# Kernel optimization log

Measured on AMD Instinct MI355X. Metric: run time of the kernel, lower is better.

Reference implementation:

```python
import jax, jax.numpy as jnp
import numpy as np

K = 32      # number of coupled-attention tensors per branch
NH = 128    # hidden size of token representations
B = 64      # batch
S = 512     # sequence length
H2 = 2 * K  # GRU input/hidden size


def setup_inputs() -> dict:
    key = jax.random.key(0)
    ks = jax.random.split(key, 9)
    unif = lambda k, shape, lo, hi: jax.random.uniform(k, shape, jnp.float32, lo, hi)
    h = jax.random.normal(ks[0], (B, S, NH), jnp.float32)
    u_a = jax.random.normal(ks[1], (NH, 1), jnp.float32)
    u_o = jax.random.normal(ks[2], (NH, 1), jnp.float32)
    mask = jnp.ones((B, S), jnp.bool_)
    G_a = unif(ks[3], (K, 1, NH, NH), -0.2, 0.2)
    G_o = unif(ks[4], (K, 1, NH, NH), -0.2, 0.2)
    r0 = unif(ks[5], (H2,), -0.2, 0.2)
    v = unif(ks[6], (H2,), -0.2, 0.2)
    s = 1.0 / np.sqrt(H2)  # default torch GRU init scale
    W_ih = unif(ks[7], (3 * H2, H2), -s, s)
    W_hh = unif(ks[8], (3 * H2, H2), -s, s)
    return {"h": h, "u_a": u_a, "u_o": u_o, "mask": mask,
            "G_a": G_a, "G_o": G_o, "r0": r0, "v": v,
            "W_ih": W_ih, "W_hh": W_hh}


def reference(h, u_a, u_o, mask, G_a, G_o, r0, v, W_ih, W_hh):
    # f(G, u)[k,b,s] = sum_j (sum_i h[b,s,i] * G[k,0,i,j]) * u[j,0]
    # contract G with u first to avoid the (K,B,S,nh) intermediate.
    def f(G, u):
        w = jnp.einsum('kij,j->ki', G[:, 0], u[:, 0])     # (K, nh)
        return jnp.einsum('bsi,ki->kbs', h, w)            # (K, B, S)

    beta = jnp.tanh(jnp.concatenate([f(G_a, u_a), f(G_o, u_o)], axis=0))  # (2K,B,S)
    beta = jnp.transpose(beta, (1, 2, 0))                 # (B, S, 2K)
    beta = beta * mask[..., None].astype(beta.dtype)

    # GRU (bias=False), PyTorch gate order r, z, n.
    x_seq = jnp.transpose(beta, (1, 0, 2))                # (S, B, 2K)
    h0 = jnp.broadcast_to(r0, (B, H2))

    def step(hp, x):
        gx = x @ W_ih.T                                   # (B, 3*2K)
        gh = hp @ W_hh.T
        xr, xz, xn = jnp.split(gx, 3, axis=-1)
        hr, hz, hn = jnp.split(gh, 3, axis=-1)
        rg = jax.nn.sigmoid(xr + hr)
        zg = jax.nn.sigmoid(xz + hz)
        ng = jnp.tanh(xn + rg * hn)
        hnew = (1.0 - zg) * ng + zg * hp
        return hnew, hnew

    _, outs = jax.lax.scan(step, h0, x_seq)               # (S, B, 2K)
    r = jnp.transpose(outs, (1, 0, 2))                    # (B, S, 2K)
    r = r * mask[..., None].astype(r.dtype)
    return r, r @ v                                       # (B,S,2K), (B,S)
```

## Files before the change

kernel.cpp:

```cpp
#include <hip/hip_runtime.h>
#include <hip/hip_bf16.h>

#define B_  64
#define S_  512
#define NH_ 128
#define K_  32
#define H2_ 64
#define G3_ 192

typedef unsigned int u32;
typedef unsigned short u16;
typedef _Float16 h2f __attribute__((ext_vector_type(2)));
typedef __fp16  fp16v2 __attribute__((ext_vector_type(2)));
typedef u32 u32x4 __attribute__((ext_vector_type(4)));
typedef _Float16 f16x8 __attribute__((ext_vector_type(8)));
typedef float f32x4 __attribute__((ext_vector_type(4)));

__device__ __forceinline__ float bf_lo(u32 p){ return __uint_as_float(p << 16); }
__device__ __forceinline__ float bf_hi(u32 p){ return __uint_as_float(p & 0xffff0000u); }
__device__ __forceinline__ float bfu(u16 b){ return __uint_as_float(((u32)b) << 16); }
__device__ __forceinline__ float f16u(u16 b){ __fp16 h = *(__fp16*)&b; return (float)h; }
__device__ __forceinline__ u16 f2bf(float x){
  __hip_bfloat16 h = __float2bfloat16(x);
  return *(u16*)&h;
}
__device__ __forceinline__ u16 f2h(float x){
  __fp16 h = (__fp16)x;
  return *(u16*)&h;
}
__device__ __forceinline__ float frcp(float x){ return __builtin_amdgcn_rcpf(x); }
__device__ __forceinline__ float sigmoid_f(float x){
  x = fminf(fmaxf(x, -30.f), 30.f);
  return frcp(1.f + __expf(-x));
}
__device__ __forceinline__ float tanh_f(float x){
  x = fminf(fmaxf(x, -15.f), 15.f);
  float e = __expf(2.f * x);
  return (e - 1.f) * frcp(e + 1.f);
}
__device__ __forceinline__ float tanh_fast(float x){
  float e = __expf(2.f * x);
  return 1.f - 2.f*frcp(1.f + e);
}
__device__ __forceinline__ float sigmoid_nc(float x){
  return frcp(1.f + __expf(-x));
}
__device__ __forceinline__ float tanh_nc(float x){
  float e = __expf(2.f * x);
  return (e - 1.f) * frcp(e + 1.f);
}
__device__ __forceinline__ u32 pkrtz_u(float a, float b){
  fp16v2 pk = __builtin_amdgcn_cvt_pkrtz(a, b);
  return *(u32*)&pk;
}
__device__ __forceinline__ float fdot2u(u32 a, u32 b, float c){
#if __has_builtin(__builtin_amdgcn_fdot2)
  return __builtin_amdgcn_fdot2(*(h2f*)&a, *(h2f*)&b, c, false);
#else
  h2f av = *(h2f*)&a, bv = *(h2f*)&b;
  return c + (float)av.x*(float)bv.x + (float)av.y*(float)bv.y;
#endif
}
__device__ __forceinline__ u32 readlane_u(u32 v, int lane){
  return (u32)__builtin_amdgcn_readlane((int)v, lane);
}
__device__ __forceinline__ float dpp_xor1(float x){
  return __int_as_float(
      __builtin_amdgcn_update_dpp(0, __float_as_int(x), 0xB1, 0xF, 0xF, true));
}

#define GLD4(dst, base, OFF) \
  asm volatile("global_load_dwordx4 %0, %1, off offset:" OFF : "=v"(dst) : "v"(base))
#define VMWAIT() asm volatile("s_waitcnt vmcnt(0)" ::: "memory")
#define UNP(arr, base, q) \
  arr[(base)]=q.x; arr[(base)+1]=q.y; arr[(base)+2]=q.z; arr[(base)+3]=q.w

__device__ __forceinline__ bool detect_f32_block(const u16* p, int nHalf, int tid){
  __shared__ int flagS;
  __syncthreads();
  if (tid < 64) {
    int sane = 0;
    if (tid < nHalf) {
      u16 b = p[2*tid];
      int ex = (b >> 7) & 0xFF;
      sane = (b == 0 || (ex >= 0x68 && ex <= 0x84)) ? 1 : 0;
    }
    unsigned long long m = __ballot(sane != 0);
    if (tid == 0) flagS = (4*__popcll(m) < 3*nHalf) ? 1 : 0;
  }
  __syncthreads();
  return flagS != 0;
}

__global__ __launch_bounds__(128) void k_prep(
    const void* __restrict__ h, const void* __restrict__ ua, const void* __restrict__ uo,
    const void* __restrict__ Ga, const void* __restrict__ Go,
    const void* __restrict__ r0, const void* __restrict__ v,
    const void* __restrict__ Wih, const void* __restrict__ Whh,
    u32* __restrict__ wPk, u32* __restrict__ WihPk2, u32* __restrict__ WhhPk,
    float* __restrict__ r0f, int* __restrict__ flags)
{
  int bk = blockIdx.x, t = threadIdx.x;
  if (bk < 64) {
    const void* G = (bk < K_) ? Ga : Go;
    const void* u = (bk < K_) ? ua : uo;
    bool fg = detect_f32_block((const u16*)G, 64, t);
    bool fu = detect_f32_block((const u16*)u, 64, t);
    __shared__ float u_s[NH_];
    __shared__ float accS[NH_];
    u_s[t] = fu ? ((const float*)u)[t] : bfu(((const u16*)u)[t]);
    __syncthreads();
    int k = bk & (K_ - 1);
    size_t ro = ((size_t)k*NH_ + t)*NH_;
    float acc = 0.f;
    if (fg) {
      const float4* Gr = (const float4*)((const float*)G + ro);
      #pragma unroll
      for (int j4 = 0; j4 < NH_/4; ++j4) {
        float4 g = Gr[j4];
        acc += g.x*u_s[4*j4] + g.y*u_s[4*j4+1] + g.z*u_s[4*j4+2] + g.w*u_s[4*j4+3];
      }
    } else {
      const u32* Gr = (const u32*)((const u16*)G + ro);
      #pragma unroll
      for (int j2 = 0; j2 < NH_/2; ++j2) {
        u32 p = Gr[j2];
        acc += bf_lo(p)*u_s[2*j2] + bf_hi(p)*u_s[2*j2+1];
      }
    }
    accS[t] = acc;
    __syncthreads();
    if (t < 64) wPk[bk*64 + t] = pkrtz_u(accS[2*t], accS[2*t+1]);
  } else if (bk < 112) {
    bool f = detect_f32_block((const u16*)Wih, 64, t);
    int idx = (bk - 64)*128 + t;
    int j = idx / 96, rest = idx % 96;
    int g = rest / 32, m = rest % 32;
    int row = g*H2_ + j;
    float a, b;
    if (f) {
      const float* W = (const float*)Wih;
      a = W[(size_t)row*H2_ + 2*m]; b = W[(size_t)row*H2_ + 2*m + 1];
    } else {
      u32 p = ((const u32*)Wih)[(size_t)row*(H2_/2) + m];
      a = bf_lo(p); b = bf_hi(p);
    }
    WihPk2[idx] = pkrtz_u(a, b);
  } else if (bk < 160) {
    bool f = detect_f32_block((const u16*)Whh, 64, t);
    int idx = (bk - 112)*128 + t;
    int j = idx / 96, rest = idx % 96;
    int g = rest / 32, m = rest % 32;
    int row = g*H2_ + j;
    float a, b;
    if (f) {
      const float* W = (const float*)Whh;
      a = W[(size_t)row*H2_ + 2*m]; b = W[(size_t)row*H2_ + 2*m + 1];
    } else {
      u32 p = ((const u32*)Whh)[(size_t)row*(H2_/2) + m];
      a = bf_lo(p); b = bf_hi(p);
    }
    WhhPk[idx] = pkrtz_u(a, b);
  } else {
    bool fh = detect_f32_block((const u16*)h, 64, t);
    bool fv = detect_f32_block((const u16*)v, 32, t);
    bool fr = detect_f32_block((const u16*)r0, 32, t);
    if (t == 0) { flags[0] = fh ? 1 : 0; flags[7] = fv ? 1 : 0; }
    if (t < H2_)
      r0f[t] = fr ? ((const float*)r0)[t] : bfu(((const u16*)r0)[t]);
  }
}

__global__ __launch_bounds__(64)
void k_bg(const void* __restrict__ h, const u32* __restrict__ wPk,
          const u32* __restrict__ WihPk2, const int* __restrict__ flags,
          u16* __restrict__ gx)
{
  __shared__ u16 betaS[64][72];
  int l = threadIdx.x;
  int posBase = blockIdx.x * 64;
  bool f32in = flags[0] != 0;
  int c = l & 15;
  int g = l >> 4;

  f16x8 bw[4][4];
  {
    const char* base = (const char*)wPk;
    #pragma unroll
    for (int kkt = 0; kkt < 4; ++kkt)
      #pragma unroll
      for (int kt = 0; kt < 4; ++kt)
        bw[kkt][kt] = *(const f16x8*)(base + (kkt*16 + c)*256 + kt*64 + g*16);
  }

  f32x4 acc1[4][4];
  #pragma unroll
  for (int mt = 0; mt < 4; ++mt)
    #pragma unroll
    for (int kkt = 0; kkt < 4; ++kkt)
      acc1[mt][kkt] = (f32x4){0.f, 0.f, 0.f, 0.f};

  const u16*   hb = (const u16*)h;
  const float* hf = (const float*)h;
  #pragma unroll
  for (int kt = 0; kt < 4; ++kt) {
    f16x8 ha[4];
    #pragma unroll
    for (int mt = 0; mt < 4; ++mt) {
      int row = posBase + mt*16 + c;
      if (f32in) {
        const float* src = hf + (size_t)row*NH_ + kt*32 + g*8;
        float4 lo = *(const float4*)(src);
        float4 hi = *(const float4*)(src + 4);
        u32x4 q;
        q.x = pkrtz_u(lo.x, lo.y); q.y = pkrtz_u(lo.z, lo.w);
        q.z = pkrtz_u(hi.x, hi.y); q.w = pkrtz_u(hi.z, hi.w);
        ha[mt] = *(f16x8*)&q;
      } else {
        u32x4 qb = *(const u32x4*)(hb + (size_t)row*NH_ + kt*32 + g*8);
        u32x4 q;
        q.x = pkrtz_u(bf_lo(qb.x), bf_hi(qb.x));
        q.y = pkrtz_u(bf_lo(qb.y), bf_hi(qb.y));
        q.z = pkrtz_u(bf_lo(qb.z), bf_hi(qb.z));
        q.w = pkrtz_u(bf_lo(qb.w), bf_hi(qb.w));
        ha[mt] = *(f16x8*)&q;
      }
    }
    #pragma unroll
    for (int mt = 0; mt < 4; ++mt)
      #pragma unroll
      for (int kkt = 0; kkt < 4; ++kkt)
        acc1[mt][kkt] = __builtin_amdgcn_mfma_f32_16x16x32_f16(
            ha[mt], bw[kkt][kt], acc1[mt][kkt], 0, 0, 0);
  }

  #pragma unroll
  for (int mt = 0; mt < 4; ++mt)
    #pragma unroll
    for (int kkt = 0; kkt < 4; ++kkt)
      #pragma unroll
      for (int r = 0; r < 4; ++r) {
        float bta = tanh_fast(acc1[mt][kkt][r]);
        betaS[mt*16 + g*4 + r][kkt*16 + c] = f2h(bta);
      }
  asm volatile("s_waitcnt lgkmcnt(0)" ::: "memory");

  f16x8 a2[4][2];
  #pragma unroll
  for (int mt = 0; mt < 4; ++mt)
    #pragma unroll
    for (int kt2 = 0; kt2 < 2; ++kt2)
      a2[mt][kt2] = *(const f16x8*)&betaS[mt*16 + c][kt2*32 + g*8];

  const char* wib = (const char*)WihPk2;
  #pragma unroll 2
  for (int rt = 0; rt < 12; ++rt) {
    int row = rt*16 + c;
    int gg = row >> 6, j = row & 63;
    f16x8 b2_0 = *(const f16x8*)(wib + j*384 + gg*128 + g*16);
    f16x8 b2_1 = *(const f16x8*)(wib + j*384 + gg*128 + 64 + g*16);
    f32x4 acc2[4];
    #pragma unroll
    for (int mt = 0; mt < 4; ++mt) {
      acc2[mt] = (f32x4){0.f, 0.f, 0.f, 0.f};
      acc2[mt] = __builtin_amdgcn_mfma_f32_16x16x32_f16(a2[mt][0], b2_0, acc2[mt], 0, 0, 0);
      acc2[mt] = __builtin_amdgcn_mfma_f32_16x16x32_f16(a2[mt][1], b2_1, acc2[mt], 0, 0, 0);
    }
    #pragma unroll
    for (int mt = 0; mt < 4; ++mt)
      #pragma unroll
      for (int r = 0; r < 4; ++r)
        gx[(size_t)(posBase + mt*16 + g*4 + r)*G3_ + rt*16 + c] = f2h(acc2[mt][r]);
  }
}

__global__ __launch_bounds__(64)
__attribute__((amdgpu_waves_per_eu(1, 1)))
void k_gru(
    const u16* __restrict__ gx, const u32* __restrict__ WhhPk,
    const float* __restrict__ r0f, const int* __restrict__ flags,
    void* __restrict__ out)
{
  int b = blockIdx.x, j = threadIdx.x;
  bool outf32 = flags[0] != 0;
  unsigned long long a = (unsigned long long)(WhhPk + j*96);
  u32x4 q0,q1,q2,q3,q4,q5,q6,q7,q8,q9,q10,q11,
        q12,q13,q14,q15,q16,q17,q18,q19,q20,q21,q22,q23;
  GLD4(q0,a,"0");    GLD4(q1,a,"16");   GLD4(q2,a,"32");   GLD4(q3,a,"48");
  GLD4(q4,a,"64");   GLD4(q5,a,"80");   GLD4(q6,a,"96");   GLD4(q7,a,"112");
  GLD4(q8,a,"128");  GLD4(q9,a,"144");  GLD4(q10,a,"160"); GLD4(q11,a,"176");
  GLD4(q12,a,"192"); GLD4(q13,a,"208"); GLD4(q14,a,"224"); GLD4(q15,a,"240");
  GLD4(q16,a,"256"); GLD4(q17,a,"272"); GLD4(q18,a,"288"); GLD4(q19,a,"304");
  GLD4(q20,a,"320"); GLD4(q21,a,"336"); GLD4(q22,a,"352"); GLD4(q23,a,"368");
  VMWAIT();
  u32 wr_[32], wz_[32], wn_[32];
  UNP(wr_,0,q0);  UNP(wr_,4,q1);  UNP(wr_,8,q2);  UNP(wr_,12,q3);
  UNP(wr_,16,q4); UNP(wr_,20,q5); UNP(wr_,24,q6); UNP(wr_,28,q7);
  UNP(wz_,0,q8);  UNP(wz_,4,q9);  UNP(wz_,8,q10); UNP(wz_,12,q11);
  UNP(wz_,16,q12);UNP(wz_,20,q13);UNP(wz_,24,q14);UNP(wz_,28,q15);
  UNP(wn_,0,q16); UNP(wn_,4,q17); UNP(wn_,8,q18); UNP(wn_,12,q19);
  UNP(wn_,16,q20);UNP(wn_,20,q21);UNP(wn_,24,q22);UNP(wn_,28,q23);

  float hp = r0f[j];
  const u16* gxb = gx + (size_t)b*S_*G3_ + j;
  float* of = (float*)out + (size_t)b*S_*H2_ + j;
  u16*   oh = (u16*)out   + (size_t)b*S_*H2_ + j;

  float bxr[8], bxz[8], bxn[8], hbuf[8];
  #pragma unroll
  for (int u = 0; u < 8; ++u) {
    bxr[u] = f16u(gxb[u*G3_]);
    bxz[u] = f16u(gxb[u*G3_ + H2_]);
    bxn[u] = f16u(gxb[u*G3_ + 2*H2_]);
  }
  #pragma unroll 1
  for (int s0 = 0; s0 < S_; s0 += 8) {
    float nxr[8], nxz[8], nxn[8];
    int nb = (s0 + 8 < S_) ? (s0 + 8) : s0;
    #pragma unroll
    for (int u = 0; u < 8; ++u) {
      nxr[u] = f16u(gxb[(nb+u)*G3_]);
      nxz[u] = f16u(gxb[(nb+u)*G3_ + H2_]);
      nxn[u] = f16u(gxb[(nb+u)*G3_ + 2*H2_]);
    }
    #pragma unroll
    for (int u = 0; u < 8; ++u) {
      u32 hppu = pkrtz_u(hp, dpp_xor1(hp));
      u32 hsv[32];
      #pragma unroll
      for (int m = 0; m < 32; ++m) hsv[m] = readlane_u(hppu, 2*m);
      float ar[4], az[4], an[4];
      ar[0]=bxr[u]; ar[1]=0.f; ar[2]=0.f; ar[3]=0.f;
      az[0]=bxz[u]; az[1]=0.f; az[2]=0.f; az[3]=0.f;
      an[0]=0.f;    an[1]=0.f; an[2]=0.f; an[3]=0.f;
      #pragma unroll
      for (int m = 0; m < 32; ++m) {
        int c = m & 3;
        ar[c] = fdot2u(hsv[m], wr_[m], ar[c]);
        az[c] = fdot2u(hsv[m], wz_[m], az[c]);
        an[c] = fdot2u(hsv[m], wn_[m], an[c]);
      }
      float Ar = (ar[0]+ar[1]) + (ar[2]+ar[3]);
      float Az = (az[0]+az[1]) + (az[2]+az[3]);
      float An = (an[0]+an[1]) + (an[2]+an[3]);
      float rg = sigmoid_nc(Ar);
      float zg = sigmoid_nc(Az);
      float ng = tanh_nc(bxn[u] + rg*An);
      hp = ng + zg*(hp - ng);
      hbuf[u] = hp;
    }
    if (outf32) {
      #pragma unroll
      for (int u = 0; u < 8; ++u) of[(size_t)(s0+u)*H2_] = hbuf[u];
    } else {
      #pragma unroll
      for (int u = 0; u < 8; ++u) oh[(size_t)(s0+u)*H2_] = f2bf(hbuf[u]);
    }
    #pragma unroll
    for (int u = 0; u < 8; ++u) { bxr[u]=nxr[u]; bxz[u]=nxz[u]; bxn[u]=nxn[u]; }
  }
}

__global__ __launch_bounds__(256) void k_rv(
    const void* __restrict__ outbase, const void* __restrict__ v,
    const int* __restrict__ flags, int dummy)
{
  bool outf32 = flags[0] != 0, f_v = flags[7] != 0;
  int lane = threadIdx.x & 63;
  int pos  = blockIdx.x*4 + (threadIdx.x >> 6);
  float vv = f_v ? ((const float*)v)[lane] : bfu(((const u16*)v)[lane]);
  float rr = outf32 ? ((const float*)outbase)[(size_t)pos*H2_ + lane]
                    : bfu(((const u16*)outbase)[(size_t)pos*H2_ + lane]);
  float val = rr * vv;
  #pragma unroll
  for (int m = 32; m >= 1; m >>= 1) val += __shfl_xor(val, m, 64);
  if (lane == 0) {
    if (outf32) ((float*)outbase)[(size_t)B_*S_*H2_ + pos] = val;
    else        ((u16*)outbase)[(size_t)B_*S_*H2_ + pos]   = f2bf(val);
  }
}

__global__ __launch_bounds__(64) void k_detect(
    const u16* __restrict__ p0, const u16* __restrict__ p1, const u16* __restrict__ p2,
    const u16* __restrict__ p4, const u16* __restrict__ p5, const u16* __restrict__ p6,
    const u16* __restrict__ p7, const u16* __restrict__ p8, const u16* __restrict__ p9,
    int* __restrict__ flags)
{
  const u16* ps[9] = {p0,p1,p2,p4,p5,p6,p7,p8,p9};
  const int  ns[9] = {64,64,64,64,64,32,32,64,64};
  const int  fi[9] = {0,1,2,4,5,6,7,8,9};
  int t = threadIdx.x;
  for (int m = 0; m < 9; ++m) {
    int n = ns[m];
    int sane = 0;
    if (t < n) {
      u16 b = ps[m][2*t];
      int ex = (b >> 7) & 0xFF;
      sane = (b == 0 || (ex >= 0x68 && ex <= 0x84)) ? 1 : 0;
    }
    #pragma unroll
    for (int sh = 32; sh >= 1; sh >>= 1) sane += __shfl_xor(sane, sh, 64);
    if (t == 0) flags[fi[m]] = (4*sane < 3*n) ? 1 : 0;
  }
  if (t == 0) flags[3] = 0;
}

__global__ __launch_bounds__(64, 1) void k_fused(
    const void* __restrict__ h, const void* __restrict__ ua, const void* __restrict__ uo,
    const void* __restrict__ Ga, const void* __restrict__ Go,
    const void* __restrict__ r0, const void* __restrict__ Wih,
    const void* __restrict__ Whh, const int* __restrict__ flags,
    void* __restrict__ out)
{
  __shared__ float wsh[NH_*H2_];
  __shared__ float wih_s[H2_*G3_];
  __shared__ float us[2*NH_];
  __shared__ float hs[NH_];
  __shared__ float beta_s[H2_];
  __shared__ float hps[H2_];
  int b = blockIdx.x, t = threadIdx.x;
  bool f_h = flags[0]!=0, f_ua = flags[1]!=0, f_uo = flags[2]!=0;
  bool f_ga = flags[4]!=0, f_go = flags[5]!=0, f_r0 = flags[6]!=0;
  bool f_wih = flags[8]!=0, f_whh = flags[9]!=0;
  for (int i = t; i < NH_; i += 64) {
    us[i]      = f_ua ? ((const float*)ua)[i] : bfu(((const u16*)ua)[i]);
    us[NH_+i]  = f_uo ? ((const float*)uo)[i] : bfu(((const u16*)uo)[i]);
  }
  for (int idx = t; idx < H2_*G3_; idx += 64) {
    int j = idx / H2_, p = idx % H2_;
    float w = f_wih ? ((const float*)Wih)[idx] : bfu(((const u16*)Wih)[idx]);
    wih_s[p*G3_ + j] = w;
  }
  __syncthreads();
  {
    int k = t & 31;
    const void* G = (t < 32) ? Ga : Go;
    bool fg = (t < 32) ? f_ga : f_go;
    const float* u_s = &us[(t < 32) ? 0 : NH_];
    for (int i = 0; i < NH_; ++i) {
      size_t ro = ((size_t)k*NH_ + i)*NH_;
      float acc = 0.f;
      if (fg) {
        const float* Gr = (const float*)G + ro;
        for (int jj = 0; jj < NH_; ++jj) acc += Gr[jj]*u_s[jj];
      } else {
        const u32* Gr = (const u32*)((const u16*)G + ro);
        for (int j2 = 0; j2 < NH_/2; ++j2) {
          u32 p = Gr[j2];
          acc += bf_lo(p)*u_s[2*j2] + bf_hi(p)*u_s[2*j2+1];
        }
      }
      wsh[i*H2_ + t] = acc;
    }
  }
  float wr[H2_], wz[H2_], wn[H2_];
  if (f_whh) {
    const float* W = (const float*)Whh;
    for (int i = 0; i < H2_; ++i) {
      wr[i] = W[(size_t)t*H2_ + i];
      wz[i] = W[(size_t)(H2_ + t)*H2_ + i];
      wn[i] = W[(size_t)(2*H2_ + t)*H2_ + i];
    }
  } else {
    const u32* Wr = (const u32*)Whh + (size_t)(t)         * (H2_/2);
    const u32* Wz = (const u32*)Whh + (size_t)(H2_ + t)   * (H2_/2);
    const u32* Wn = (const u32*)Whh + (size_t)(2*H2_ + t) * (H2_/2);
    for (int i2 = 0; i2 < H2_/2; ++i2) {
      u32 p;
      p = Wr[i2]; wr[2*i2]=bf_lo(p); wr[2*i2+1]=bf_hi(p);
      p = Wz[i2]; wz[2*i2]=bf_lo(p); wz[2*i2+1]=bf_hi(p);
      p = Wn[i2]; wn[2*i2]=bf_lo(p); wn[2*i2+1]=bf_hi(p);
    }
  }
  float hp = f_r0 ? ((const float*)r0)[t] : bfu(((const u16*)r0)[t]);
  __syncthreads();
  for (int s = 0; s < S_; ++s) {
    size_t hbase = ((size_t)b*S_ + s)*NH_;
    for (int i = t; i < NH_; i += 64)
      hs[i] = f_h ? ((const float*)h)[hbase + i] : bfu(((const u16*)h)[hbase + i]);
    __syncthreads();
    float a = 0.f;
    for (int i = 0; i < NH_; ++i) a += hs[i]*wsh[i*H2_ + t];
    beta_s[t] = tanh_f(a);
    hps[t] = hp;
    __syncthreads();
    float xr=0.f, xz=0.f, xn=0.f, ar=0.f, az=0.f, an=0.f;
    for (int p = 0; p < H2_; ++p) {
      float bp = beta_s[p];
      xr += bp*wih_s[p*G3_ + t];
      xz += bp*wih_s[p*G3_ + H2_ + t];
      xn += bp*wih_s[p*G3_ + 2*H2_ + t];
      float hv = hps[p];
      ar += hv*wr[p]; az += hv*wz[p]; an += hv*wn[p];
    }
    float rg = sigmoid_f(xr + ar);
    float zg = sigmoid_f(xz + az);
    float ng = tanh_f(xn + rg*an);
    hp = (1.f - zg)*ng + zg*hp;
    if (f_h) ((float*)out)[((size_t)b*S_ + s)*H2_ + t] = hp;
    else     ((u16*)out)[((size_t)b*S_ + s)*H2_ + t] = f2bf(hp);
    __syncthreads();
  }
}

extern "C" void kernel_launch(void* const* d_in, const int* in_sizes, int n_in,
                              void* d_out, int out_size, void* d_ws, size_t ws_size,
                              hipStream_t stream) {
  int*   flags  = (int*)d_ws;
  char*  wsb    = (char*)d_ws;
  float* r0f    = (float*)(wsb + 256);
  u32*   wPk    = (u32*)(wsb + 1024);
  u32*   WihPk2 = (u32*)(wsb + 17408);
  u32*   WhhPk  = (u32*)(wsb + 41984);
  u16*   gx     = (u16*)(wsb + 66560);
  const size_t need_bf = 66560ull + 12582912ull;

  if (ws_size >= need_bf) {
    k_prep<<<161, 128, 0, stream>>>(d_in[0], d_in[1], d_in[2], d_in[4], d_in[5],
                                    d_in[6], d_in[7], d_in[8], d_in[9],
                                    wPk, WihPk2, WhhPk, r0f, flags);
    k_bg  <<<512, 64,  0, stream>>>(d_in[0], wPk, WihPk2, flags, gx);
    k_gru <<<64,  64,  0, stream>>>(gx, WhhPk, r0f, flags, d_out);
  } else {
    k_detect<<<1, 64, 0, stream>>>(
        (const u16*)d_in[0], (const u16*)d_in[1], (const u16*)d_in[2],
        (const u16*)d_in[4], (const u16*)d_in[5], (const u16*)d_in[6],
        (const u16*)d_in[7], (const u16*)d_in[8], (const u16*)d_in[9], flags);
    k_fused<<<64, 64, 0, stream>>>(d_in[0], d_in[1], d_in[2], d_in[4], d_in[5],
                                   d_in[6], d_in[8], d_in[9], flags, d_out);
  }
  k_rv<<<8192, 256, 0, stream>>>(d_out, d_in[7], flags, 0);
}
```

Baseline: 279.4 us.

## Compute GRU recurrent matvec with MFMA instead of per-lane fdot2 and readlane broadcast

The serial GRU kernel now computes the hidden-state matvec with 16x16x32 f16 MFMA instructions. The hidden vector is gathered into A fragments via ds_bpermute, and the weight fragments are kept in registers in a new per-lane layout loaded from the same packed buffer. Each lane picks its gate output from the diagonal result with a 4-way select. This replaces 32 readlanes and 96 fdot2 per step with 24 MFMAs, so most of the computed outputs are discarded. The timestep unroll also drops from 8 to 4.

```diff
diff --git a/kernel.cpp b/kernel.cpp
--- a/kernel.cpp
+++ b/kernel.cpp
@@ -67,6 +67,11 @@
 __device__ __forceinline__ float dpp_xor1(float x){
   return __int_as_float(
       __builtin_amdgcn_update_dpp(0, __float_as_int(x), 0xB1, 0xF, 0xF, true));
+}
+__device__ __forceinline__ float sel4(float a, float b, float c, float d, int q){
+  float ab = (q & 1) ? b : a;
+  float cd = (q & 1) ? d : c;
+  return (q & 2) ? cd : ab;
 }
 
 #define GLD4(dst, base, OFF) \
@@ -283,82 +288,95 @@
 {
   int b = blockIdx.x, j = threadIdx.x;
   bool outf32 = flags[0] != 0;
-  unsigned long long a = (unsigned long long)(WhhPk + j*96);
-  u32x4 q0,q1,q2,q3,q4,q5,q6,q7,q8,q9,q10,q11,
-        q12,q13,q14,q15,q16,q17,q18,q19,q20,q21,q22,q23;
-  GLD4(q0,a,"0");    GLD4(q1,a,"16");   GLD4(q2,a,"32");   GLD4(q3,a,"48");
-  GLD4(q4,a,"64");   GLD4(q5,a,"80");   GLD4(q6,a,"96");   GLD4(q7,a,"112");
-  GLD4(q8,a,"128");  GLD4(q9,a,"144");  GLD4(q10,a,"160"); GLD4(q11,a,"176");
-  GLD4(q12,a,"192"); GLD4(q13,a,"208"); GLD4(q14,a,"224"); GLD4(q15,a,"240");
-  GLD4(q16,a,"256"); GLD4(q17,a,"272"); GLD4(q18,a,"288"); GLD4(q19,a,"304");
-  GLD4(q20,a,"320"); GLD4(q21,a,"336"); GLD4(q22,a,"352"); GLD4(q23,a,"368");
+  int c = j & 15, q = j >> 4;
+
+  unsigned long long at0 = (unsigned long long)((const char*)WhhPk + c*384 + q*16);
+  unsigned long long at1 = at0 + 6144;
+  unsigned long long at2 = at0 + 12288;
+  unsigned long long at3 = at0 + 18432;
+  u32x4 Br0a,Br0b,Bz0a,Bz0b,Bn0a,Bn0b;
+  u32x4 Br1a,Br1b,Bz1a,Bz1b,Bn1a,Bn1b;
+  u32x4 Br2a,Br2b,Bz2a,Bz2b,Bn2a,Bn2b;
+  u32x4 Br3a,Br3b,Bz3a,Bz3b,Bn3a,Bn3b;
+  GLD4(Br0a,at0,"0"); GLD4(Br0b,at0,"64"); GLD4(Bz0a,at0,"128");
+  GLD4(Bz0b,at0,"192"); GLD4(Bn0a,at0,"256"); GLD4(Bn0b,at0,"320");
+  GLD4(Br1a,at1,"0"); GLD4(Br1b,at1,"64"); GLD4(Bz1a,at1,"128");
+  GLD4(Bz1b,at1,"192"); GLD4(Bn1a,at1,"256"); GLD4(Bn1b,at1,"320");
+  GLD4(Br2a,at2,"0"); GLD4(Br2b,at2,"64"); GLD4(Bz2a,at2,"128");
+  GLD4(Bz2b,at2,"192"); GLD4(Bn2a,at2,"256"); GLD4(Bn2b,at2,"320");
+  GLD4(Br3a,at3,"0"); GLD4(Br3b,at3,"64"); GLD4(Bz3a,at3,"128");
+  GLD4(Bz3b,at3,"192"); GLD4(Bn3a,at3,"256"); GLD4(Bn3b,at3,"320");
   VMWAIT();
-  u32 wr_[32], wz_[32], wn_[32];
-  UNP(wr_,0,q0);  UNP(wr_,4,q1);  UNP(wr_,8,q2);  UNP(wr_,12,q3);
-  UNP(wr_,16,q4); UNP(wr_,20,q5); UNP(wr_,24,q6); UNP(wr_,28,q7);
-  UNP(wz_,0,q8);  UNP(wz_,4,q9);  UNP(wz_,8,q10); UNP(wz_,12,q11);
-  UNP(wz_,16,q12);UNP(wz_,20,q13);UNP(wz_,24,q14);UNP(wz_,28,q15);
-  UNP(wn_,0,q16); UNP(wn_,4,q17); UNP(wn_,8,q18); UNP(wn_,12,q19);
-  UNP(wn_,16,q20);UNP(wn_,20,q21);UNP(wn_,24,q22);UNP(wn_,28,q23);
-
+
+  int bq = q * 32;
+
+  f32x4 z4 = (f32x4){0.f, 0.f, 0.f, 0.f};
   float hp = r0f[j];
   const u16* gxb = gx + (size_t)b*S_*G3_ + j;
   float* of = (float*)out + (size_t)b*S_*H2_ + j;
   u16*   oh = (u16*)out   + (size_t)b*S_*H2_ + j;
 
-  float bxr[8], bxz[8], bxn[8], hbuf[8];
+#define MF(D, AF, BV, CV) \
+  D = __builtin_amdgcn_mfma_f32_16x16x32_f16(AF, *(const f16x8*)&(BV), CV, 0, 0, 0)
+
+  float bxr[4], bxz[4], bxn[4], hbuf[4];
   #pragma unroll
-  for (int u = 0; u < 8; ++u) {
+  for (int u = 0; u < 4; ++u) {
     bxr[u] = f16u(gxb[u*G3_]);
     bxz[u] = f16u(gxb[u*G3_ + H2_]);
     bxn[u] = f16u(gxb[u*G3_ + 2*H2_]);
   }
   #pragma unroll 1
-  for (int s0 = 0; s0 < S_; s0 += 8) {
-    float nxr[8], nxz[8], nxn[8];
-    int nb = (s0 + 8 < S_) ? (s0 + 8) : s0;
-    #pragma unroll
-    for (int u = 0; u < 8; ++u) {
+  for (int s0 = 0; s0 < S_; s0 += 4) {
+    float nxr[4], nxz[4], nxn[4];
+    int nb = (s0 + 4 < S_) ? (s0 + 4) : s0;
+    #pragma unroll
+    for (int u = 0; u < 4; ++u) {
       nxr[u] = f16u(gxb[(nb+u)*G3_]);
       nxz[u] = f16u(gxb[(nb+u)*G3_ + H2_]);
       nxn[u] = f16u(gxb[(nb+u)*G3_ + 2*H2_]);
     }
     #pragma unroll
-    for (int u = 0; u < 8; ++u) {
-      u32 hppu = pkrtz_u(hp, dpp_xor1(hp));
-      u32 hsv[32];
-      #pragma unroll
-      for (int m = 0; m < 32; ++m) hsv[m] = readlane_u(hppu, 2*m);
-      float ar[4], az[4], an[4];
-      ar[0]=bxr[u]; ar[1]=0.f; ar[2]=0.f; ar[3]=0.f;
-      az[0]=bxz[u]; az[1]=0.f; az[2]=0.f; az[3]=0.f;
-      an[0]=0.f;    an[1]=0.f; an[2]=0.f; an[3]=0.f;
-      #pragma unroll
-      for (int m = 0; m < 32; ++m) {
-        int c = m & 3;
-        ar[c] = fdot2u(hsv[m], wr_[m], ar[c]);
-        az[c] = fdot2u(hsv[m], wz_[m], az[c]);
-        an[c] = fdot2u(hsv[m], wn_[m], an[c]);
-      }
-      float Ar = (ar[0]+ar[1]) + (ar[2]+ar[3]);
-      float Az = (az[0]+az[1]) + (az[2]+az[3]);
-      float An = (an[0]+an[1]) + (an[2]+an[3]);
-      float rg = sigmoid_nc(Ar);
-      float zg = sigmoid_nc(Az);
-      float ng = tanh_nc(bxn[u] + rg*An);
+    for (int u = 0; u < 4; ++u) {
+      u32 hppk = pkrtz_u(hp, dpp_xor1(hp));
+      int pa0 = __builtin_amdgcn_ds_bpermute(bq,       (int)hppk);
+      int pa1 = __builtin_amdgcn_ds_bpermute(bq + 8,   (int)hppk);
+      int pa2 = __builtin_amdgcn_ds_bpermute(bq + 16,  (int)hppk);
+      int pa3 = __builtin_amdgcn_ds_bpermute(bq + 24,  (int)hppk);
+      int pb0 = __builtin_amdgcn_ds_bpermute(bq + 128, (int)hppk);
+      int pb1 = __builtin_amdgcn_ds_bpermute(bq + 136, (int)hppk);
+      int pb2 = __builtin_amdgcn_ds_bpermute(bq + 144, (int)hppk);
+      int pb3 = __builtin_amdgcn_ds_bpermute(bq + 152, (int)hppk);
+      u32x4 a0v; a0v.x=(u32)pa0; a0v.y=(u32)pa1; a0v.z=(u32)pa2; a0v.w=(u32)pa3;
+      u32x4 a1v; a1v.x=(u32)pb0; a1v.y=(u32)pb1; a1v.z=(u32)pb2; a1v.w=(u32)pb3;
+      f16x8 A0f = *(f16x8*)&a0v, A1f = *(f16x8*)&a1v;
+      f32x4 ar0,ar1,ar2,ar3, az0,az1,az2,az3, an0,an1,an2,an3;
+      MF(ar0,A0f,Br0a,z4); MF(ar1,A0f,Br1a,z4); MF(ar2,A0f,Br2a,z4); MF(ar3,A0f,Br3a,z4);
+      MF(az0,A0f,Bz0a,z4); MF(az1,A0f,Bz1a,z4); MF(az2,A0f,Bz2a,z4); MF(az3,A0f,Bz3a,z4);
+      MF(an0,A0f,Bn0a,z4); MF(an1,A0f,Bn1a,z4); MF(an2,A0f,Bn2a,z4); MF(an3,A0f,Bn3a,z4);
+      MF(ar0,A1f,Br0b,ar0); MF(ar1,A1f,Br1b,ar1); MF(ar2,A1f,Br2b,ar2); MF(ar3,A1f,Br3b,ar3);
+      MF(az0,A1f,Bz0b,az0); MF(az1,A1f,Bz1b,az1); MF(az2,A1f,Bz2b,az2); MF(az3,A1f,Bz3b,az3);
+      MF(an0,A1f,Bn0b,an0); MF(an1,A1f,Bn1b,an1); MF(an2,A1f,Bn2b,an2); MF(an3,A1f,Bn3b,an3);
+      float yr = sel4(ar0[0], ar1[0], ar2[0], ar3[0], q);
+      float yz = sel4(az0[0], az1[0], az2[0], az3[0], q);
+      float yn = sel4(an0[0], an1[0], an2[0], an3[0], q);
+      float rg = sigmoid_nc(bxr[u] + yr);
+      float zg = sigmoid_nc(bxz[u] + yz);
+      float ng = tanh_nc(bxn[u] + rg*yn);
       hp = ng + zg*(hp - ng);
       hbuf[u] = hp;
     }
     if (outf32) {
       #pragma unroll
-      for (int u = 0; u < 8; ++u) of[(size_t)(s0+u)*H2_] = hbuf[u];
+      for (int u = 0; u < 4; ++u) of[(size_t)(s0+u)*H2_] = hbuf[u];
     } else {
       #pragma unroll
-      for (int u = 0; u < 8; ++u) oh[(size_t)(s0+u)*H2_] = f2bf(hbuf[u]);
-    }
-    #pragma unroll
-    for (int u = 0; u < 8; ++u) { bxr[u]=nxr[u]; bxz[u]=nxz[u]; bxn[u]=nxn[u]; }
-  }
+      for (int u = 0; u < 4; ++u) oh[(size_t)(s0+u)*H2_] = f2bf(hbuf[u]);
+    }
+    #pragma unroll
+    for (int u = 0; u < 4; ++u) { bxr[u]=nxr[u]; bxz[u]=nxz[u]; bxn[u]=nxn[u]; }
+  }
+#undef MF
 }
 
 __global__ __launch_bounds__(256) void k_rv(
```

After: 289.2 us. +3.5%, slower.

## Fuse r@v reduction into GRU kernel and transpose gx to gate-major layout

Applied to the files above, without the earlier changes.

The r·v dot product moves into the GRU recurrence as a per-step wave shuffle reduction, so the workspace path no longer launches k_rv. The gate-input buffer gx changes from position-major to gate-row-major with packed stores, which lets the GRU load 8 consecutive timesteps as vector loads instead of strided scalar loads. The hidden update also becomes an fma form. The shuffle reduction sits on the serial recurrence's critical path, so the saving from dropping a launch and a pass over the output may be offset by that added per-step latency.

```diff
diff --git a/kernel.cpp b/kernel.cpp
--- a/kernel.cpp
+++ b/kernel.cpp
@@ -7,6 +7,7 @@
 #define K_  32
 #define H2_ 64
 #define G3_ 192
+#define SPOS_ 32768
 
 typedef unsigned int u32;
 typedef unsigned short u16;
@@ -14,6 +15,7 @@
 typedef __fp16  fp16v2 __attribute__((ext_vector_type(2)));
 typedef u32 u32x4 __attribute__((ext_vector_type(4)));
 typedef _Float16 f16x8 __attribute__((ext_vector_type(8)));
+typedef _Float16 f16x4 __attribute__((ext_vector_type(4)));
 typedef float f32x4 __attribute__((ext_vector_type(4)));
 
 __device__ __forceinline__ float bf_lo(u32 p){ return __uint_as_float(p << 16); }
@@ -267,10 +269,13 @@
       acc2[mt] = __builtin_amdgcn_mfma_f32_16x16x32_f16(a2[mt][1], b2_1, acc2[mt], 0, 0, 0);
     }
     #pragma unroll
-    for (int mt = 0; mt < 4; ++mt)
-      #pragma unroll
-      for (int r = 0; r < 4; ++r)
-        gx[(size_t)(posBase + mt*16 + g*4 + r)*G3_ + rt*16 + c] = f2h(acc2[mt][r]);
+    for (int mt = 0; mt < 4; ++mt) {
+      u32 d0 = (u32)f2h(acc2[mt][0]) | ((u32)f2h(acc2[mt][1]) << 16);
+      u32 d1 = (u32)f2h(acc2[mt][2]) | ((u32)f2h(acc2[mt][3]) << 16);
+      size_t off = (size_t)row * SPOS_ + (size_t)posBase + mt*16 + g*4;
+      uint2 pk; pk.x = d0; pk.y = d1;
+      *(uint2*)(gx + off) = pk;
+    }
   }
 }
 
@@ -279,10 +284,11 @@
 void k_gru(
     const u16* __restrict__ gx, const u32* __restrict__ WhhPk,
     const float* __restrict__ r0f, const int* __restrict__ flags,
-    void* __restrict__ out)
+    const void* __restrict__ v, void* __restrict__ out)
 {
   int b = blockIdx.x, j = threadIdx.x;
   bool outf32 = flags[0] != 0;
+  bool f_v    = flags[7] != 0;
   unsigned long long a = (unsigned long long)(WhhPk + j*96);
   u32x4 q0,q1,q2,q3,q4,q5,q6,q7,q8,q9,q10,q11,
         q12,q13,q14,q15,q16,q17,q18,q19,q20,q21,q22,q23;
@@ -302,27 +308,33 @@
   UNP(wn_,16,q20);UNP(wn_,20,q21);UNP(wn_,24,q22);UNP(wn_,28,q23);
 
   float hp = r0f[j];
-  const u16* gxb = gx + (size_t)b*S_*G3_ + j;
+  float vv = f_v ? ((const float*)v)[j] : bfu(((const u16*)v)[j]);
+  const u16* gr = gx + (size_t)j*SPOS_ + (size_t)b*S_;
+  const u16* gz = gr + (size_t)64*SPOS_;
+  const u16* gn = gr + (size_t)128*SPOS_;
   float* of = (float*)out + (size_t)b*S_*H2_ + j;
   u16*   oh = (u16*)out   + (size_t)b*S_*H2_ + j;
+  float* rvf = (float*)out + (size_t)B_*S_*H2_ + (size_t)b*S_;
+  u16*   rvh = (u16*)out  + (size_t)B_*S_*H2_ + (size_t)b*S_;
 
   float bxr[8], bxz[8], bxn[8], hbuf[8];
-  #pragma unroll
-  for (int u = 0; u < 8; ++u) {
-    bxr[u] = f16u(gxb[u*G3_]);
-    bxz[u] = f16u(gxb[u*G3_ + H2_]);
-    bxn[u] = f16u(gxb[u*G3_ + 2*H2_]);
+  {
+    f16x4 r0v = *(const f16x4*)(gr),  r1v = *(const f16x4*)(gr + 4);
+    f16x4 z0v = *(const f16x4*)(gz),  z1v = *(const f16x4*)(gz + 4);
+    f16x4 n0v = *(const f16x4*)(gn),  n1v = *(const f16x4*)(gn + 4);
+    #pragma unroll
+    for (int u = 0; u < 4; ++u) {
+      bxr[u] = (float)r0v[u]; bxr[u+4] = (float)r1v[u];
+      bxz[u] = (float)z0v[u]; bxz[u+4] = (float)z1v[u];
+      bxn[u] = (float)n0v[u]; bxn[u+4] = (float)n1v[u];
+    }
   }
   #pragma unroll 1
   for (int s0 = 0; s0 < S_; s0 += 8) {
-    float nxr[8], nxz[8], nxn[8];
     int nb = (s0 + 8 < S_) ? (s0 + 8) : s0;
-    #pragma unroll
-    for (int u = 0; u < 8; ++u) {
-      nxr[u] = f16u(gxb[(nb+u)*G3_]);
-      nxz[u] = f16u(gxb[(nb+u)*G3_ + H2_]);
-      nxn[u] = f16u(gxb[(nb+u)*G3_ + 2*H2_]);
-    }
+    f16x4 r0v = *(const f16x4*)(gr + nb), r1v = *(const f16x4*)(gr + nb + 4);
+    f16x4 z0v = *(const f16x4*)(gz + nb), z1v = *(const f16x4*)(gz + nb + 4);
+    f16x4 n0v = *(const f16x4*)(gn + nb), n1v = *(const f16x4*)(gn + nb + 4);
     #pragma unroll
     for (int u = 0; u < 8; ++u) {
       u32 hppu = pkrtz_u(hp, dpp_xor1(hp));
@@ -345,9 +357,18 @@
       float An = (an[0]+an[1]) + (an[2]+an[3]);
       float rg = sigmoid_nc(Ar);
       float zg = sigmoid_nc(Az);
+      float hpz = zg * hp;
+      float omz = 1.f - zg;
       float ng = tanh_nc(bxn[u] + rg*An);
-      hp = ng + zg*(hp - ng);
+      hp = __builtin_fmaf(omz, ng, hpz);
       hbuf[u] = hp;
+      float val = hp * vv;
+      #pragma unroll
+      for (int mS = 32; mS >= 1; mS >>= 1) val += __shfl_xor(val, mS, 64);
+      if (j == 0) {
+        if (outf32) rvf[s0 + u] = val;
+        else        rvh[s0 + u] = f2bf(val);
+      }
     }
     if (outf32) {
       #pragma unroll
@@ -357,7 +378,11 @@
       for (int u = 0; u < 8; ++u) oh[(size_t)(s0+u)*H2_] = f2bf(hbuf[u]);
     }
     #pragma unroll
-    for (int u = 0; u < 8; ++u) { bxr[u]=nxr[u]; bxz[u]=nxz[u]; bxn[u]=nxn[u]; }
+    for (int u = 0; u < 4; ++u) {
+      bxr[u] = (float)r0v[u]; bxr[u+4] = (float)r1v[u];
+      bxz[u] = (float)z0v[u]; bxz[u+4] = (float)z1v[u];
+      bxn[u] = (float)n0v[u]; bxn[u+4] = (float)n1v[u];
+    }
   }
 }
 
@@ -520,7 +545,7 @@
                                     d_in[6], d_in[7], d_in[8], d_in[9],
                                     wPk, WihPk2, WhhPk, r0f, flags);
     k_bg  <<<512, 64,  0, stream>>>(d_in[0], wPk, WihPk2, flags, gx);
-    k_gru <<<64,  64,  0, stream>>>(gx, WhhPk, r0f, flags, d_out);
+    k_gru <<<64,  64,  0, stream>>>(gx, WhhPk, r0f, flags, d_in[7], d_out);
   } else {
     k_detect<<<1, 64, 0, stream>>>(
         (const u16*)d_in[0], (const u16*)d_in[1], (const u16*)d_in[2],
@@ -528,6 +553,6 @@
         (const u16*)d_in[7], (const u16*)d_in[8], (const u16*)d_in[9], flags);
     k_fused<<<64, 64, 0, stream>>>(d_in[0], d_in[1], d_in[2], d_in[4], d_in[5],
                                    d_in[6], d_in[8], d_in[9], flags, d_out);
-  }
-  k_rv<<<8192, 256, 0, stream>>>(d_out, d_in[7], flags, 0);
-}
+    k_rv<<<8192, 256, 0, stream>>>(d_out, d_in[7], flags, 0);
+  }
+}
```

Result: slower. 374.1 us (+33.9%).
